# Kernel optimization log

Hardware: AMD Instinct MI355X
Metric: run time of the kernel (lower is better)

Reference implementation:

```python
import jax, jax.numpy as jnp
import numpy as np

N_HEADS = 8


def setup_inputs() -> dict:
    key = jax.random.key(0)
    qkv = jax.random.normal(key, (4, 1536, 2048), dtype=jnp.float32)
    return {"qkv": qkv}


def reference(qkv) -> jnp.ndarray:
    bs, width, length = qkv.shape
    assert width % (3 * N_HEADS) == 0
    ch = width // (3 * N_HEADS)
    # [bs*H, 3*ch, T] -> split into q, k, v each [bs*H, ch, T]
    qkv_ = qkv.reshape(bs * N_HEADS, 3 * ch, length)
    q, k, v = qkv_[:, :ch], qkv_[:, ch:2 * ch], qkv_[:, 2 * ch:]
    scale = 1.0 / np.sqrt(np.sqrt(ch)).astype(np.float32)
    # scores [bs*H, T_q, T_k]
    weight = jnp.einsum('bct,bcs->bts', q * scale, k * scale)
    # NOTE: faithful to source — softmax over dim=1 (the query axis t), in float32
    weight = jax.nn.softmax(weight.astype(jnp.float32), axis=1).astype(weight.dtype)
    a = jnp.einsum('bts,bcs->bct', weight, v)  # [bs*H, ch, T]
    return a.reshape(bs, N_HEADS * ch, length)
```

## Files before the change

kernel.cpp:

```cpp
#include <hip/hip_runtime.h>
#include <hip/hip_bf16.h>


#define SEQ   2048
#define CHD   64
#define NHB   32
#define SCALE_QK 0.42466090f

typedef short bf16x8 __attribute__((ext_vector_type(8)));
typedef float f32x4  __attribute__((ext_vector_type(4)));
typedef float f32x16 __attribute__((ext_vector_type(16)));
typedef unsigned int   u32x4 __attribute__((ext_vector_type(4)));
typedef unsigned short us8   __attribute__((ext_vector_type(8)));

extern "C" __device__ float __ocml_native_exp2_f32(float);
#define EXP2(x) __ocml_native_exp2_f32(x)

__device__ __forceinline__ unsigned short f2bf(float f) {
    unsigned int u = __builtin_bit_cast(unsigned int, f);
    u += 0x7FFFu + ((u >> 16) & 1u);
    return (unsigned short)(u >> 16);
}

__device__ __forceinline__ void gl_lds16(const void* g, void* l) {
    __builtin_amdgcn_global_load_lds(
        (const __attribute__((address_space(1))) void*)g,
        (__attribute__((address_space(3))) void*)l, 16, 0, 0);
}

__device__ __forceinline__ unsigned cvtpk(float a, float b) {
    unsigned r;
    asm("v_cvt_pk_bf16_f32 %0, %1, %2" : "=v"(r) : "v"(a), "v"(b));
    return r;
}
__device__ __forceinline__ void plswap(unsigned &a, unsigned &b) {
    asm("v_permlane32_swap_b32 %0, %1" : "+v"(a), "+v"(b));
}

#define ZERO16 {0.f,0.f,0.f,0.f,0.f,0.f,0.f,0.f,0.f,0.f,0.f,0.f,0.f,0.f,0.f,0.f}

__global__ __launch_bounds__(256) void convert_qk(
    const float* __restrict__ qkv, unsigned short* __restrict__ Qt,
    unsigned short* __restrict__ Kt)
{
    __shared__ float Tl[64][129];
    const int bid = blockIdx.x;
    const int head = bid >> 4, t0 = (bid & 15) * 128;
    const int b = head >> 3, h = head & 7;
    const float* base = qkv + (size_t)(b * 1536 + h * 192) * SEQ;
    const int tid = threadIdx.x;
#pragma unroll
    for (int pp = 0; pp < 2; ++pp) {
        const float* src = base + (size_t)(pp ? CHD : 0) * SEQ;
        unsigned short* dst = (pp ? Kt : Qt) + (size_t)head * SEQ * CHD;
        if (pp) __syncthreads();
        for (int e = tid; e < 8192; e += 256) {
            int c = e >> 7, ti = e & 127;
            Tl[c][ti] = src[(size_t)c * SEQ + t0 + ti];
        }
        __syncthreads();
        for (int g = tid; g < 1024; g += 256) {
            int t = g >> 3, cg = g & 7;
            us8 u;
#pragma unroll
            for (int j = 0; j < 8; ++j) u[j] = f2bf(Tl[cg * 8 + j][t] * SCALE_QK);
            *(us8*)(dst + (size_t)(t0 + t) * 64 + ((cg * 8) ^ ((t & 7) << 3))) = u;
        }
    }
}

__global__ __launch_bounds__(512, 2) void stats10_kernel(
    const float* __restrict__ qkv, const unsigned short* __restrict__ Qt,
    const unsigned short* __restrict__ Kt, unsigned short* __restrict__ Vb)
{
    __shared__ __attribute__((aligned(16))) unsigned short Qs[4][4096];
    __shared__ float rlb[256];
    const int bid = blockIdx.x;
    const int bs  = ((bid & 7) << 5) | (bid >> 3);
    const int head = bs >> 3, s0 = (bs & 7) * 256;
    const int b = head >> 3, h = head & 7;
    const char* Qhb = (const char*)(Qt + (size_t)head * SEQ * CHD);
    const unsigned short* Kh = Kt + (size_t)head * SEQ * CHD;
    const int tid = threadIdx.x, w = tid >> 6, l = tid & 63, lo5 = l & 31, hi = l >> 5;
    const int rsw = (lo5 & 7) << 3;

    bf16x8 kfr[4];
#pragma unroll
    for (int kc = 0; kc < 4; ++kc)
        kfr[kc] = *(const bf16x8*)(
            Kh + (size_t)(s0 + w * 32 + lo5) * 64 + (((kc << 4) + (hi << 3)) ^ rsw));

    auto stage = [&](int p, int tc) {
        gl_lds16(Qhb + (size_t)tc * 8192 + tid * 16, &Qs[p][0] + tid * 8);
    };

    float lacc[4] = {0.f, 0.f, 0.f, 0.f};

    stage(0, 0);
    stage(1, 1);
    for (int tc = 0; tc < 32; ++tc) {
        if (tc < 31) asm volatile("s_waitcnt vmcnt(1)" ::: "memory");
        else         asm volatile("s_waitcnt vmcnt(0)" ::: "memory");
        __builtin_amdgcn_s_barrier();
        __builtin_amdgcn_sched_barrier(0);
        if (tc < 30) stage((tc + 2) & 3, tc + 2);
        const unsigned short* qs = &Qs[tc & 3][0];
        __builtin_amdgcn_s_setprio(1);
#pragma unroll
        for (int ts = 0; ts < 2; ++ts) {
            f32x16 s = ZERO16;
#pragma unroll
            for (int kc = 0; kc < 4; ++kc) {
                bf16x8 qa = *(const bf16x8*)(
                    qs + (ts * 32 + lo5) * 64 + (((kc << 4) + (hi << 3)) ^ rsw));
                s = __builtin_amdgcn_mfma_f32_32x32x16_bf16(qa, kfr[kc], s, 0, 0, 0);
            }
#pragma unroll
            for (int r = 0; r < 16; ++r) lacc[r & 3] += EXP2(s[r]);
        }
        __builtin_amdgcn_s_setprio(0);
    }

    float lsum = (lacc[0] + lacc[1]) + (lacc[2] + lacc[3]);
    lsum += __shfl_xor(lsum, 32);
    if (l < 32) rlb[w * 32 + lo5] = 1.0f / lsum;
    __syncthreads();

    const float* vp = qkv + (size_t)(b * 1536 + h * 192 + 2 * CHD) * SEQ;
    unsigned short* Vh = Vb + (size_t)head * SEQ * CHD;
    for (int g = tid; g < 2048; g += 512) {
        int c = g >> 5, si8 = (g & 31) * 8;
        const float* vrow = vp + (size_t)c * SEQ + s0 + si8;
        f32x4 v0 = *(const f32x4*)(vrow);
        f32x4 v1 = *(const f32x4*)(vrow + 4);
        us8 u;
#pragma unroll
        for (int j = 0; j < 4; ++j) u[j]     = f2bf(v0[j] * rlb[si8 + j]);
#pragma unroll
        for (int j = 0; j < 4; ++j) u[4 + j] = f2bf(v1[j] * rlb[si8 + 4 + j]);
        int swb = (si8 & ~63) | ((si8 & 63) ^ ((c & 7) << 3));
        *(us8*)(Vh + (size_t)c * SEQ + s0 + swb) = u;
    }
}

__global__ __launch_bounds__(512, 2) void attn8_kernel(
    const unsigned short* __restrict__ Qt, const unsigned short* __restrict__ Kt,
    const unsigned short* __restrict__ Vb, float* __restrict__ out)
{
    __shared__ __attribute__((aligned(16))) unsigned short KV[4][8192];
    const int bid = blockIdx.x;
    const int bs  = ((bid & 7) << 5) | (bid >> 3);
    const int head = bs >> 3, t0 = (bs & 7) * 256;
    const int b = head >> 3, h = head & 7;
    const int tid = threadIdx.x, w = tid >> 6, l = tid & 63, lo5 = l & 31, hi = l >> 5;
    const int rsw = (lo5 & 7) << 3;
    const unsigned short* Qh = Qt + (size_t)head * SEQ * CHD;
    const char* Khb = (const char*)(Kt + (size_t)head * SEQ * CHD);
    const char* Vhb = (const char*)(Vb + (size_t)head * SEQ * CHD);
    const int tmine = t0 + w * 32 + lo5;

    bf16x8 qf[4];
#pragma unroll
    for (int kc = 0; kc < 4; ++kc)
        qf[kc] = *(const bf16x8*)(Qh + (size_t)tmine * 64 + (((kc << 4) + (hi << 3)) ^ rsw));

    f32x16 acc[2] = {ZERO16, ZERO16};

    const int vc = tid >> 3, vs16 = (tid & 7) * 16;
    auto stage = [&](int p, int cj) {
        unsigned short* kb = &KV[p][0];
        unsigned short* vb = &KV[p][4096];
        gl_lds16(Khb + (size_t)cj * 8192 + tid * 16, kb + tid * 8);
        gl_lds16(Vhb + (size_t)vc * 4096 + (size_t)cj * 128 + vs16,
                 vb + tid * 8);
    };

    stage(0, 0);
    stage(1, 1);

    for (int j = 0; j < 32; ++j) {
        const int p = j & 3;
        if (j < 31) asm volatile("s_waitcnt vmcnt(2)" ::: "memory");
        else        asm volatile("s_waitcnt vmcnt(0)" ::: "memory");
        __builtin_amdgcn_s_barrier();
        __builtin_amdgcn_sched_barrier(0);
        if (j < 30) stage((j + 2) & 3, j + 2);

        const unsigned short* kb = &KV[p][0];
        const unsigned short* vb = &KV[p][4096];
        bf16x8 vf[8];
#pragma unroll
        for (int ct = 0; ct < 2; ++ct)
#pragma unroll
            for (int ks = 0; ks < 4; ++ks)
                vf[ct * 4 + ks] = *(const bf16x8*)(
                    vb + (ct * 32 + lo5) * 64 + (((ks << 4) + (hi << 3)) ^ rsw));

        __builtin_amdgcn_s_setprio(1);
#pragma unroll
        for (int st = 0; st < 2; ++st) {
            f32x16 sacc = ZERO16;
#pragma unroll
            for (int kc = 0; kc < 4; ++kc) {
                bf16x8 kf = *(const bf16x8*)(
                    kb + (st * 32 + lo5) * 64 + (((kc << 4) + (hi << 3)) ^ rsw));
                sacc = __builtin_amdgcn_mfma_f32_32x32x16_bf16(kf, qf[kc], sacc, 0, 0, 0);
            }
            float p16[16];
#pragma unroll
            for (int r = 0; r < 16; ++r) p16[r] = EXP2(sacc[r]);
            unsigned w0 = cvtpk(p16[0],  p16[1]),  w1 = cvtpk(p16[2],  p16[3]);
            unsigned w2 = cvtpk(p16[4],  p16[5]),  w3 = cvtpk(p16[6],  p16[7]);
            unsigned w4 = cvtpk(p16[8],  p16[9]),  w5 = cvtpk(p16[10], p16[11]);
            unsigned w6 = cvtpk(p16[12], p16[13]), w7 = cvtpk(p16[14], p16[15]);
            plswap(w0, w2); plswap(w1, w3); plswap(w4, w6); plswap(w5, w7);
            bf16x8 pfA = __builtin_bit_cast(bf16x8, (u32x4){w0, w1, w2, w3});
            bf16x8 pfB = __builtin_bit_cast(bf16x8, (u32x4){w4, w5, w6, w7});
#pragma unroll
            for (int ct = 0; ct < 2; ++ct) {
                acc[ct] = __builtin_amdgcn_mfma_f32_32x32x16_bf16(vf[ct * 4 + st * 2 + 0], pfA, acc[ct], 0, 0, 0);
                acc[ct] = __builtin_amdgcn_mfma_f32_32x32x16_bf16(vf[ct * 4 + st * 2 + 1], pfB, acc[ct], 0, 0, 0);
            }
        }
        __builtin_amdgcn_s_setprio(0);
    }

    float* op = out + (size_t)(b * 512 + h * 64) * SEQ;
#pragma unroll
    for (int ct = 0; ct < 2; ++ct)
#pragma unroll
        for (int r = 0; r < 16; ++r) {
            int c = ct * 32 + (r & 3) + 8 * (r >> 2) + 4 * hi;
            op[(size_t)c * SEQ + tmine] = acc[ct][r];
        }
}


__device__ __forceinline__ bf16x8 lds_frag(const unsigned short* base, int row, int el) {
    int e = el ^ ((row & 7) << 3);
    return *(const bf16x8*)(base + row * 64 + e);
}

__global__ __launch_bounds__(256) void qkv_stats_kernel(
    const float* __restrict__ qkv, float* __restrict__ m_ws, float* __restrict__ rl_ws)
{
    __shared__ __attribute__((aligned(16))) unsigned short Kl[128 * 64];
    __shared__ __attribute__((aligned(16))) unsigned short Ql[64 * 64];
    const int head = blockIdx.x >> 4, stile = blockIdx.x & 15, s0 = stile * 128;
    const int b = head >> 3, h = head & 7;
    const float* qp = qkv + (size_t)(b * 1536 + h * 192) * SEQ;
    const float* kp = qp + (size_t)CHD * SEQ;
    const int tid = threadIdx.x, w = tid >> 6, l = tid & 63, lg = l >> 4, lr = l & 15;
    for (int idx = tid; idx < 128 * 64; idx += 256) {
        int s = idx & 127, c = idx >> 7;
        Kl[s * 64 + (c ^ ((s & 7) << 3))] = f2bf(kp[(size_t)c * SEQ + s0 + s]);
    }
    float m_run[2] = {-__builtin_inff(), -__builtin_inff()};
    float l_run[2] = {0.f, 0.f};
    for (int chunk = 0; chunk < 32; ++chunk) {
        const int t0 = chunk * 64;
        __syncthreads();
        for (int idx = tid; idx < 64 * 64; idx += 256) {
            int t = idx & 63, c = idx >> 6;
            Ql[t * 64 + (c ^ ((t & 7) << 3))] = f2bf(qp[(size_t)c * SEQ + t0 + t]);
        }
        __syncthreads();
#pragma unroll
        for (int ntl = 0; ntl < 2; ++ntl) {
            const int srow = 16 * (2 * w + ntl) + lr;
            float vals[16];
#pragma unroll
            for (int mt = 0; mt < 4; ++mt) {
                f32x4 sacc = {0.f, 0.f, 0.f, 0.f};
#pragma unroll
                for (int kk = 0; kk < 2; ++kk) {
                    bf16x8 a  = lds_frag(Ql, 16 * mt + lr, 32 * kk + 8 * lg);
                    bf16x8 bk = lds_frag(Kl, srow,         32 * kk + 8 * lg);
                    sacc = __builtin_amdgcn_mfma_f32_16x16x32_bf16(a, bk, sacc, 0, 0, 0);
                }
#pragma unroll
                for (int j = 0; j < 4; ++j) vals[mt * 4 + j] = sacc[j] * 0.125f;
            }
            float cm = vals[0];
#pragma unroll
            for (int i = 1; i < 16; ++i) cm = fmaxf(cm, vals[i]);
            cm = fmaxf(cm, __shfl_xor(cm, 16));
            cm = fmaxf(cm, __shfl_xor(cm, 32));
            float newm = fmaxf(m_run[ntl], cm);
            l_run[ntl] *= __expf(m_run[ntl] - newm);
            m_run[ntl] = newm;
            float ps = 0.f;
#pragma unroll
            for (int i = 0; i < 16; ++i) ps += __expf(vals[i] - newm);
            ps += __shfl_xor(ps, 16);
            ps += __shfl_xor(ps, 32);
            l_run[ntl] += ps;
        }
    }
    if (lg == 0) {
#pragma unroll
        for (int ntl = 0; ntl < 2; ++ntl) {
            int sg = s0 + 16 * (2 * w + ntl) + lr;
            m_ws[head * SEQ + sg]  = m_run[ntl];
            rl_ws[head * SEQ + sg] = 1.0f / l_run[ntl];
        }
    }
}

__global__ __launch_bounds__(256) void qkv_attn_kernel(
    const float* __restrict__ qkv, const float* __restrict__ m_ws,
    const float* __restrict__ rl_ws, float* __restrict__ out)
{
    __shared__ __attribute__((aligned(16))) unsigned short Ql[128 * 64];
    __shared__ __attribute__((aligned(16))) unsigned short Kl[64 * 64];
    __shared__ __attribute__((aligned(16))) unsigned short Vl[64 * 64];
    __shared__ __attribute__((aligned(16))) unsigned short Pl[128 * 64];
    const int head = blockIdx.x >> 4, ttile = blockIdx.x & 15, t0 = ttile * 128;
    const int b = head >> 3, h = head & 7;
    const float* qp  = qkv + (size_t)(b * 1536 + h * 192) * SEQ;
    const float* kp  = qp + (size_t)CHD * SEQ;
    const float* vp  = qp + (size_t)(2 * CHD) * SEQ;
    const float* mh  = m_ws  + head * SEQ;
    const float* rlh = rl_ws + head * SEQ;
    const int tid = threadIdx.x, w = tid >> 6, l = tid & 63, lg = l >> 4, lr = l & 15;
    for (int idx = tid; idx < 128 * 64; idx += 256) {
        int t = idx & 127, c = idx >> 7;
        Ql[t * 64 + (c ^ ((t & 7) << 3))] = f2bf(qp[(size_t)c * SEQ + t0 + t]);
    }
    f32x4 acc[4][2];
#pragma unroll
    for (int i = 0; i < 4; ++i)
#pragma unroll
        for (int j = 0; j < 2; ++j) acc[i][j] = (f32x4){0.f, 0.f, 0.f, 0.f};
    for (int sc = 0; sc < 32; ++sc) {
        const int s0 = sc * 64;
        __syncthreads();
        for (int idx = tid; idx < 64 * 64; idx += 256) {
            int s = idx & 63, c = idx >> 6;
            Kl[s * 64 + (c ^ ((s & 7) << 3))] = f2bf(kp[(size_t)c * SEQ + s0 + s]);
            Vl[c * 64 + (s ^ ((c & 7) << 3))] = f2bf(vp[(size_t)c * SEQ + s0 + s] * rlh[s0 + s]);
        }
        __syncthreads();
        float msv[4];
#pragma unroll
        for (int nts = 0; nts < 4; ++nts) msv[nts] = mh[s0 + 16 * nts + lr];
#pragma unroll
        for (int mts = 0; mts < 2; ++mts) {
            const int trowbase = 16 * (2 * w + mts);
#pragma unroll
            for (int nts = 0; nts < 4; ++nts) {
                f32x4 sa = {0.f, 0.f, 0.f, 0.f};
#pragma unroll
                for (int kk = 0; kk < 2; ++kk) {
                    bf16x8 a  = lds_frag(Ql, trowbase + lr, 32 * kk + 8 * lg);
                    bf16x8 bk = lds_frag(Kl, 16 * nts + lr, 32 * kk + 8 * lg);
                    sa = __builtin_amdgcn_mfma_f32_16x16x32_bf16(a, bk, sa, 0, 0, 0);
                }
                const int scol = 16 * nts + lr;
#pragma unroll
                for (int j = 0; j < 4; ++j) {
                    int trow = trowbase + 4 * lg + j;
                    float p = __expf(sa[j] * 0.125f - msv[nts]);
                    Pl[trow * 64 + (scol ^ ((trow & 7) << 3))] = f2bf(p);
                }
            }
        }
#pragma unroll
        for (int mt = 0; mt < 4; ++mt) {
#pragma unroll
            for (int ntl = 0; ntl < 2; ++ntl) {
                const int trow = 16 * (2 * w + ntl);
#pragma unroll
                for (int kk = 0; kk < 2; ++kk) {
                    bf16x8 a  = lds_frag(Vl, 16 * mt + lr, 32 * kk + 8 * lg);
                    bf16x8 bp = lds_frag(Pl, trow + lr,    32 * kk + 8 * lg);
                    acc[mt][ntl] = __builtin_amdgcn_mfma_f32_16x16x32_bf16(a, bp, acc[mt][ntl], 0, 0, 0);
                }
            }
        }
    }
    float* op = out + (size_t)(b * 512 + h * 64) * SEQ;
#pragma unroll
    for (int mt = 0; mt < 4; ++mt) {
#pragma unroll
        for (int ntl = 0; ntl < 2; ++ntl) {
            int tcol = t0 + 16 * (2 * w + ntl) + lr;
#pragma unroll
            for (int j = 0; j < 4; ++j) {
                int c = 16 * mt + 4 * lg + j;
                op[(size_t)c * SEQ + tcol] = acc[mt][ntl][j];
            }
        }
    }
}

extern "C" void kernel_launch(void* const* d_in, const int* in_sizes, int n_in,
                              void* d_out, int out_size, void* d_ws, size_t ws_size,
                              hipStream_t stream) {
    const float* qkv = (const float*)d_in[0];
    float* out = (float*)d_out;
    (void)in_sizes; (void)n_in; (void)out_size;

    const size_t need = (size_t)3 * NHB * SEQ * CHD * 2;
    if (ws_size >= need) {
        unsigned short* Qt = (unsigned short*)d_ws;
        unsigned short* Kt = Qt + (size_t)NHB * SEQ * CHD;
        unsigned short* Vb = Kt + (size_t)NHB * SEQ * CHD;
        convert_qk    <<<dim3(NHB * 16), dim3(256), 0, stream>>>(qkv, Qt, Kt);
        stats10_kernel<<<dim3(256),      dim3(512), 0, stream>>>(qkv, Qt, Kt, Vb);
        attn8_kernel  <<<dim3(NHB * 8),  dim3(512), 0, stream>>>(Qt, Kt, Vb, out);
    } else {
        float* m_ws  = (float*)d_ws;
        float* rl_ws = m_ws + (size_t)NHB * SEQ;
        qkv_stats_kernel<<<dim3(NHB * 16), dim3(256), 0, stream>>>(qkv, m_ws, rl_ws);
        qkv_attn_kernel <<<dim3(NHB * 16), dim3(256), 0, stream>>>(qkv, m_ws, rl_ws, out);
    }
}
```

Measured before the change: 85.05 us.

## Split key chunk across wave pairs with two query tiles per wave and LDS reduction

Each wave now handles two 32-query tiles and half of every 64-key chunk, instead of one query tile and the full chunk. K fragments are reused across both query tiles and each wave loads only half the V fragments, cutting LDS reads per MFMA. Partial P·V accumulators from each wave pair are summed through LDS at the end. Launch bounds drop to one block per CU to make room for the extra accumulators and Q fragments, which may reduce occupancy and latency hiding.

```diff
diff --git a/kernel.cpp b/kernel.cpp
--- a/kernel.cpp
+++ b/kernel.cpp
@@ -143,7 +143,7 @@
     }
 }
 
-__global__ __launch_bounds__(512, 2) void attn8_kernel(
+__global__ __launch_bounds__(512, 1) void attn13_kernel(
     const unsigned short* __restrict__ Qt, const unsigned short* __restrict__ Kt,
     const unsigned short* __restrict__ Vb, float* __restrict__ out)
 {
@@ -153,26 +153,29 @@
     const int head = bs >> 3, t0 = (bs & 7) * 256;
     const int b = head >> 3, h = head & 7;
     const int tid = threadIdx.x, w = tid >> 6, l = tid & 63, lo5 = l & 31, hi = l >> 5;
+    const int tw = w >> 1, sh = w & 1;
     const int rsw = (lo5 & 7) << 3;
     const unsigned short* Qh = Qt + (size_t)head * SEQ * CHD;
     const char* Khb = (const char*)(Kt + (size_t)head * SEQ * CHD);
     const char* Vhb = (const char*)(Vb + (size_t)head * SEQ * CHD);
-    const int tmine = t0 + w * 32 + lo5;
-
-    bf16x8 qf[4];
-#pragma unroll
-    for (int kc = 0; kc < 4; ++kc)
-        qf[kc] = *(const bf16x8*)(Qh + (size_t)tmine * 64 + (((kc << 4) + (hi << 3)) ^ rsw));
-
-    f32x16 acc[2] = {ZERO16, ZERO16};
+
+    bf16x8 qfA[4], qfB[4];
+#pragma unroll
+    for (int kc = 0; kc < 4; ++kc) {
+        qfA[kc] = *(const bf16x8*)(
+            Qh + (size_t)(t0 + tw * 64 + lo5) * 64 + (((kc << 4) + (hi << 3)) ^ rsw));
+        qfB[kc] = *(const bf16x8*)(
+            Qh + (size_t)(t0 + tw * 64 + 32 + lo5) * 64 + (((kc << 4) + (hi << 3)) ^ rsw));
+    }
+
+    f32x16 accA0 = ZERO16, accA1 = ZERO16, accB0 = ZERO16, accB1 = ZERO16;
 
     const int vc = tid >> 3, vs16 = (tid & 7) * 16;
     auto stage = [&](int p, int cj) {
         unsigned short* kb = &KV[p][0];
         unsigned short* vb = &KV[p][4096];
         gl_lds16(Khb + (size_t)cj * 8192 + tid * 16, kb + tid * 8);
-        gl_lds16(Vhb + (size_t)vc * 4096 + (size_t)cj * 128 + vs16,
-                 vb + tid * 8);
+        gl_lds16(Vhb + (size_t)vc * 4096 + (size_t)cj * 128 + vs16, vb + tid * 8);
     };
 
     stage(0, 0);
@@ -188,27 +191,30 @@
 
         const unsigned short* kb = &KV[p][0];
         const unsigned short* vb = &KV[p][4096];
-        bf16x8 vf[8];
-#pragma unroll
-        for (int ct = 0; ct < 2; ++ct)
-#pragma unroll
-            for (int ks = 0; ks < 4; ++ks)
-                vf[ct * 4 + ks] = *(const bf16x8*)(
-                    vb + (ct * 32 + lo5) * 64 + (((ks << 4) + (hi << 3)) ^ rsw));
+
+        bf16x8 kf[4], vf0k0, vf0k1, vf1k0, vf1k1;
+#pragma unroll
+        for (int kc = 0; kc < 4; ++kc)
+            kf[kc] = *(const bf16x8*)(
+                kb + (sh * 32 + lo5) * 64 + (((kc << 4) + (hi << 3)) ^ rsw));
+        vf0k0 = *(const bf16x8*)(vb + (lo5) * 64       + ((sh * 32 +      (hi << 3)) ^ rsw));
+        vf0k1 = *(const bf16x8*)(vb + (lo5) * 64       + ((sh * 32 + 16 + (hi << 3)) ^ rsw));
+        vf1k0 = *(const bf16x8*)(vb + (32 + lo5) * 64  + ((sh * 32 +      (hi << 3)) ^ rsw));
+        vf1k1 = *(const bf16x8*)(vb + (32 + lo5) * 64  + ((sh * 32 + 16 + (hi << 3)) ^ rsw));
 
         __builtin_amdgcn_s_setprio(1);
-#pragma unroll
-        for (int st = 0; st < 2; ++st) {
-            f32x16 sacc = ZERO16;
-#pragma unroll
-            for (int kc = 0; kc < 4; ++kc) {
-                bf16x8 kf = *(const bf16x8*)(
-                    kb + (st * 32 + lo5) * 64 + (((kc << 4) + (hi << 3)) ^ rsw));
-                sacc = __builtin_amdgcn_mfma_f32_32x32x16_bf16(kf, qf[kc], sacc, 0, 0, 0);
-            }
+        f32x16 SA = ZERO16, SB = ZERO16;
+#pragma unroll
+        for (int kc = 0; kc < 4; ++kc)
+            SA = __builtin_amdgcn_mfma_f32_32x32x16_bf16(kf[kc], qfA[kc], SA, 0, 0, 0);
+#pragma unroll
+        for (int kc = 0; kc < 4; ++kc)
+            SB = __builtin_amdgcn_mfma_f32_32x32x16_bf16(kf[kc], qfB[kc], SB, 0, 0, 0);
+
+        {
             float p16[16];
 #pragma unroll
-            for (int r = 0; r < 16; ++r) p16[r] = EXP2(sacc[r]);
+            for (int r = 0; r < 16; ++r) p16[r] = EXP2(SA[r]);
             unsigned w0 = cvtpk(p16[0],  p16[1]),  w1 = cvtpk(p16[2],  p16[3]);
             unsigned w2 = cvtpk(p16[4],  p16[5]),  w3 = cvtpk(p16[6],  p16[7]);
             unsigned w4 = cvtpk(p16[8],  p16[9]),  w5 = cvtpk(p16[10], p16[11]);
@@ -216,23 +222,54 @@
             plswap(w0, w2); plswap(w1, w3); plswap(w4, w6); plswap(w5, w7);
             bf16x8 pfA = __builtin_bit_cast(bf16x8, (u32x4){w0, w1, w2, w3});
             bf16x8 pfB = __builtin_bit_cast(bf16x8, (u32x4){w4, w5, w6, w7});
-#pragma unroll
-            for (int ct = 0; ct < 2; ++ct) {
-                acc[ct] = __builtin_amdgcn_mfma_f32_32x32x16_bf16(vf[ct * 4 + st * 2 + 0], pfA, acc[ct], 0, 0, 0);
-                acc[ct] = __builtin_amdgcn_mfma_f32_32x32x16_bf16(vf[ct * 4 + st * 2 + 1], pfB, acc[ct], 0, 0, 0);
-            }
+            accA0 = __builtin_amdgcn_mfma_f32_32x32x16_bf16(vf0k0, pfA, accA0, 0, 0, 0);
+            accA0 = __builtin_amdgcn_mfma_f32_32x32x16_bf16(vf0k1, pfB, accA0, 0, 0, 0);
+            accA1 = __builtin_amdgcn_mfma_f32_32x32x16_bf16(vf1k0, pfA, accA1, 0, 0, 0);
+            accA1 = __builtin_amdgcn_mfma_f32_32x32x16_bf16(vf1k1, pfB, accA1, 0, 0, 0);
+        }
+        {
+            float p16[16];
+#pragma unroll
+            for (int r = 0; r < 16; ++r) p16[r] = EXP2(SB[r]);
+            unsigned w0 = cvtpk(p16[0],  p16[1]),  w1 = cvtpk(p16[2],  p16[3]);
+            unsigned w2 = cvtpk(p16[4],  p16[5]),  w3 = cvtpk(p16[6],  p16[7]);
+            unsigned w4 = cvtpk(p16[8],  p16[9]),  w5 = cvtpk(p16[10], p16[11]);
+            unsigned w6 = cvtpk(p16[12], p16[13]), w7 = cvtpk(p16[14], p16[15]);
+            plswap(w0, w2); plswap(w1, w3); plswap(w4, w6); plswap(w5, w7);
+            bf16x8 pfA = __builtin_bit_cast(bf16x8, (u32x4){w0, w1, w2, w3});
+            bf16x8 pfB = __builtin_bit_cast(bf16x8, (u32x4){w4, w5, w6, w7});
+            accB0 = __builtin_amdgcn_mfma_f32_32x32x16_bf16(vf0k0, pfA, accB0, 0, 0, 0);
+            accB0 = __builtin_amdgcn_mfma_f32_32x32x16_bf16(vf0k1, pfB, accB0, 0, 0, 0);
+            accB1 = __builtin_amdgcn_mfma_f32_32x32x16_bf16(vf1k0, pfA, accB1, 0, 0, 0);
+            accB1 = __builtin_amdgcn_mfma_f32_32x32x16_bf16(vf1k1, pfB, accB1, 0, 0, 0);
         }
         __builtin_amdgcn_s_setprio(0);
     }
 
+    __syncthreads();
+    float* red = (float*)&KV[0][0];
+    if (sh == 0) {
+        *(f32x16*)(red + (size_t)w * 2048 + l * 16)        = accA1;
+        *(f32x16*)(red + (size_t)w * 2048 + 1024 + l * 16) = accB1;
+    } else {
+        *(f32x16*)(red + (size_t)w * 2048 + l * 16)        = accA0;
+        *(f32x16*)(red + (size_t)w * 2048 + 1024 + l * 16) = accB0;
+    }
+    __syncthreads();
+    f32x16 pA = *(const f32x16*)(red + (size_t)(w ^ 1) * 2048 + l * 16);
+    f32x16 pB = *(const f32x16*)(red + (size_t)(w ^ 1) * 2048 + 1024 + l * 16);
+    f32x16 finA, finB;
+    if (sh == 0) { finA = accA0 + pA; finB = accB0 + pB; }
+    else         { finA = accA1 + pA; finB = accB1 + pB; }
+
     float* op = out + (size_t)(b * 512 + h * 64) * SEQ;
-#pragma unroll
-    for (int ct = 0; ct < 2; ++ct)
-#pragma unroll
-        for (int r = 0; r < 16; ++r) {
-            int c = ct * 32 + (r & 3) + 8 * (r >> 2) + 4 * hi;
-            op[(size_t)c * SEQ + tmine] = acc[ct][r];
-        }
+    const int tA = t0 + tw * 64 + lo5, tB = tA + 32;
+#pragma unroll
+    for (int r = 0; r < 16; ++r) {
+        int c = sh * 32 + (r & 3) + 8 * (r >> 2) + 4 * hi;
+        op[(size_t)c * SEQ + tA] = finA[r];
+        op[(size_t)c * SEQ + tB] = finB[r];
+    }
 }
 
 
@@ -408,7 +445,7 @@
         unsigned short* Vb = Kt + (size_t)NHB * SEQ * CHD;
         convert_qk    <<<dim3(NHB * 16), dim3(256), 0, stream>>>(qkv, Qt, Kt);
         stats10_kernel<<<dim3(256),      dim3(512), 0, stream>>>(qkv, Qt, Kt, Vb);
-        attn8_kernel  <<<dim3(NHB * 8),  dim3(512), 0, stream>>>(Qt, Kt, Vb, out);
+        attn13_kernel <<<dim3(256),      dim3(512), 0, stream>>>(Qt, Kt, Vb, out);
     } else {
         float* m_ws  = (float*)d_ws;
         float* rl_ws = m_ws + (size_t)NHB * SEQ;
```

New measurement: 82.80 us (median of 3 runs). 2.6% less time.

## Split stats and attention work across twice as many blocks with atomic/LDS reductions

Applied to the files above, without the earlier changes.

The column-sum stats kernel is split into two halves over the query axis, with partial sums combined via atomic adds into a zeroed workspace. A separate small kernel then applies the reciprocal and converts V to bf16. The attention kernel now uses 128-query tiles with waves splitting the key chunk in two, reducing partial outputs through LDS. This doubles the grid size to fill more CUs, at the cost of an extra memset, an extra launch, atomics and a final LDS reduction.

```diff
diff --git a/kernel.cpp b/kernel.cpp
--- a/kernel.cpp
+++ b/kernel.cpp
@@ -69,66 +69,78 @@
     }
 }
 
-__global__ __launch_bounds__(512, 2) void stats10_kernel(
-    const float* __restrict__ qkv, const unsigned short* __restrict__ Qt,
-    const unsigned short* __restrict__ Kt, unsigned short* __restrict__ Vb)
+__global__ __launch_bounds__(512, 4) void statsA_kernel(
+    const unsigned short* __restrict__ Qt, const unsigned short* __restrict__ Kt,
+    float* __restrict__ l_ws)
 {
     __shared__ __attribute__((aligned(16))) unsigned short Qs[4][4096];
+    const int bid = blockIdx.x;
+    const int bs  = ((bid & 7) << 6) | (bid >> 3);
+    const int head = bs >> 4, s0 = ((bs >> 1) & 7) * 256, tH = bs & 1;
+    const char* Qhb = (const char*)(Qt + (size_t)head * SEQ * CHD);
+    const unsigned short* Kh = Kt + (size_t)head * SEQ * CHD;
+    const int tid = threadIdx.x, w = tid >> 6, l = tid & 63, lo5 = l & 31, hi = l >> 5;
+    const int rsw = (lo5 & 7) << 3;
+
+    bf16x8 kfr[4];
+#pragma unroll
+    for (int kc = 0; kc < 4; ++kc)
+        kfr[kc] = *(const bf16x8*)(
+            Kh + (size_t)(s0 + w * 32 + lo5) * 64 + (((kc << 4) + (hi << 3)) ^ rsw));
+
+    auto stage = [&](int p, int tc) {
+        gl_lds16(Qhb + (size_t)(tH * 16 + tc) * 8192 + tid * 16, &Qs[p][0] + tid * 8);
+    };
+
+    float lacc[4] = {0.f, 0.f, 0.f, 0.f};
+
+    stage(0, 0);
+    stage(1, 1);
+    for (int tc = 0; tc < 16; ++tc) {
+        if (tc < 15) asm volatile("s_waitcnt vmcnt(1)" ::: "memory");
+        else         asm volatile("s_waitcnt vmcnt(0)" ::: "memory");
+        __builtin_amdgcn_s_barrier();
+        __builtin_amdgcn_sched_barrier(0);
+        if (tc < 14) stage((tc + 2) & 3, tc + 2);
+        const unsigned short* qs = &Qs[tc & 3][0];
+        __builtin_amdgcn_s_setprio(1);
+#pragma unroll
+        for (int ts = 0; ts < 2; ++ts) {
+            f32x16 s = ZERO16;
+#pragma unroll
+            for (int kc = 0; kc < 4; ++kc) {
+                bf16x8 qa = *(const bf16x8*)(
+                    qs + (ts * 32 + lo5) * 64 + (((kc << 4) + (hi << 3)) ^ rsw));
+                s = __builtin_amdgcn_mfma_f32_32x32x16_bf16(qa, kfr[kc], s, 0, 0, 0);
+            }
+#pragma unroll
+            for (int r = 0; r < 16; ++r) lacc[r & 3] += EXP2(s[r]);
+        }
+        __builtin_amdgcn_s_setprio(0);
+    }
+
+    float lsum = (lacc[0] + lacc[1]) + (lacc[2] + lacc[3]);
+    lsum += __shfl_xor(lsum, 32);
+    if (l < 32) unsafeAtomicAdd(&l_ws[head * SEQ + s0 + w * 32 + lo5], lsum);
+}
+
+__global__ __launch_bounds__(256) void statsB_kernel(
+    const float* __restrict__ qkv, const float* __restrict__ l_ws,
+    unsigned short* __restrict__ Vb)
+{
     __shared__ float rlb[256];
     const int bid = blockIdx.x;
     const int bs  = ((bid & 7) << 5) | (bid >> 3);
     const int head = bs >> 3, s0 = (bs & 7) * 256;
     const int b = head >> 3, h = head & 7;
-    const char* Qhb = (const char*)(Qt + (size_t)head * SEQ * CHD);
-    const unsigned short* Kh = Kt + (size_t)head * SEQ * CHD;
-    const int tid = threadIdx.x, w = tid >> 6, l = tid & 63, lo5 = l & 31, hi = l >> 5;
-    const int rsw = (lo5 & 7) << 3;
-
-    bf16x8 kfr[4];
-#pragma unroll
-    for (int kc = 0; kc < 4; ++kc)
-        kfr[kc] = *(const bf16x8*)(
-            Kh + (size_t)(s0 + w * 32 + lo5) * 64 + (((kc << 4) + (hi << 3)) ^ rsw));
-
-    auto stage = [&](int p, int tc) {
-        gl_lds16(Qhb + (size_t)tc * 8192 + tid * 16, &Qs[p][0] + tid * 8);
-    };
-
-    float lacc[4] = {0.f, 0.f, 0.f, 0.f};
-
-    stage(0, 0);
-    stage(1, 1);
-    for (int tc = 0; tc < 32; ++tc) {
-        if (tc < 31) asm volatile("s_waitcnt vmcnt(1)" ::: "memory");
-        else         asm volatile("s_waitcnt vmcnt(0)" ::: "memory");
-        __builtin_amdgcn_s_barrier();
-        __builtin_amdgcn_sched_barrier(0);
-        if (tc < 30) stage((tc + 2) & 3, tc + 2);
-        const unsigned short* qs = &Qs[tc & 3][0];
-        __builtin_amdgcn_s_setprio(1);
-#pragma unroll
-        for (int ts = 0; ts < 2; ++ts) {
-            f32x16 s = ZERO16;
-#pragma unroll
-            for (int kc = 0; kc < 4; ++kc) {
-                bf16x8 qa = *(const bf16x8*)(
-                    qs + (ts * 32 + lo5) * 64 + (((kc << 4) + (hi << 3)) ^ rsw));
-                s = __builtin_amdgcn_mfma_f32_32x32x16_bf16(qa, kfr[kc], s, 0, 0, 0);
-            }
-#pragma unroll
-            for (int r = 0; r < 16; ++r) lacc[r & 3] += EXP2(s[r]);
-        }
-        __builtin_amdgcn_s_setprio(0);
-    }
-
-    float lsum = (lacc[0] + lacc[1]) + (lacc[2] + lacc[3]);
-    lsum += __shfl_xor(lsum, 32);
-    if (l < 32) rlb[w * 32 + lo5] = 1.0f / lsum;
+    const int tid = threadIdx.x;
+
+    rlb[tid] = 1.0f / l_ws[head * SEQ + s0 + tid];
     __syncthreads();
 
     const float* vp = qkv + (size_t)(b * 1536 + h * 192 + 2 * CHD) * SEQ;
     unsigned short* Vh = Vb + (size_t)head * SEQ * CHD;
-    for (int g = tid; g < 2048; g += 512) {
+    for (int g = tid; g < 2048; g += 256) {
         int c = g >> 5, si8 = (g & 31) * 8;
         const float* vrow = vp + (size_t)c * SEQ + s0 + si8;
         f32x4 v0 = *(const f32x4*)(vrow);
@@ -143,21 +155,22 @@
     }
 }
 
-__global__ __launch_bounds__(512, 2) void attn8_kernel(
+__global__ __launch_bounds__(512, 4) void attn9x_kernel(
     const unsigned short* __restrict__ Qt, const unsigned short* __restrict__ Kt,
     const unsigned short* __restrict__ Vb, float* __restrict__ out)
 {
-    __shared__ __attribute__((aligned(16))) unsigned short KV[4][8192];
+    __shared__ __attribute__((aligned(16))) unsigned short KV[3][8192];
     const int bid = blockIdx.x;
-    const int bs  = ((bid & 7) << 5) | (bid >> 3);
-    const int head = bs >> 3, t0 = (bs & 7) * 256;
+    const int bs  = ((bid & 7) << 6) | (bid >> 3);
+    const int head = bs >> 4, t0 = (bs & 15) * 128;
     const int b = head >> 3, h = head & 7;
     const int tid = threadIdx.x, w = tid >> 6, l = tid & 63, lo5 = l & 31, hi = l >> 5;
+    const int tsub = w >> 1, sh = w & 1;
     const int rsw = (lo5 & 7) << 3;
     const unsigned short* Qh = Qt + (size_t)head * SEQ * CHD;
     const char* Khb = (const char*)(Kt + (size_t)head * SEQ * CHD);
     const char* Vhb = (const char*)(Vb + (size_t)head * SEQ * CHD);
-    const int tmine = t0 + w * 32 + lo5;
+    const int tmine = t0 + tsub * 32 + lo5;
 
     bf16x8 qf[4];
 #pragma unroll
@@ -171,68 +184,71 @@
         unsigned short* kb = &KV[p][0];
         unsigned short* vb = &KV[p][4096];
         gl_lds16(Khb + (size_t)cj * 8192 + tid * 16, kb + tid * 8);
-        gl_lds16(Vhb + (size_t)vc * 4096 + (size_t)cj * 128 + vs16,
-                 vb + tid * 8);
+        gl_lds16(Vhb + (size_t)vc * 4096 + (size_t)cj * 128 + vs16, vb + tid * 8);
     };
 
     stage(0, 0);
     stage(1, 1);
 
     for (int j = 0; j < 32; ++j) {
-        const int p = j & 3;
+        const int p = j % 3;
         if (j < 31) asm volatile("s_waitcnt vmcnt(2)" ::: "memory");
         else        asm volatile("s_waitcnt vmcnt(0)" ::: "memory");
         __builtin_amdgcn_s_barrier();
         __builtin_amdgcn_sched_barrier(0);
-        if (j < 30) stage((j + 2) & 3, j + 2);
+        if (j < 30) stage((j + 2) % 3, j + 2);
 
         const unsigned short* kb = &KV[p][0];
         const unsigned short* vb = &KV[p][4096];
-        bf16x8 vf[8];
+        bf16x8 kf[4], vf[4];
+#pragma unroll
+        for (int kc = 0; kc < 4; ++kc)
+            kf[kc] = *(const bf16x8*)(
+                kb + (sh * 32 + lo5) * 64 + (((kc << 4) + (hi << 3)) ^ rsw));
 #pragma unroll
         for (int ct = 0; ct < 2; ++ct)
 #pragma unroll
-            for (int ks = 0; ks < 4; ++ks)
-                vf[ct * 4 + ks] = *(const bf16x8*)(
-                    vb + (ct * 32 + lo5) * 64 + (((ks << 4) + (hi << 3)) ^ rsw));
+            for (int ks = 0; ks < 2; ++ks)
+                vf[ct * 2 + ks] = *(const bf16x8*)(
+                    vb + (ct * 32 + lo5) * 64 +
+                    (((sh * 32 + ks * 16 + (hi << 3))) ^ rsw));
 
         __builtin_amdgcn_s_setprio(1);
-#pragma unroll
-        for (int st = 0; st < 2; ++st) {
-            f32x16 sacc = ZERO16;
-#pragma unroll
-            for (int kc = 0; kc < 4; ++kc) {
-                bf16x8 kf = *(const bf16x8*)(
-                    kb + (st * 32 + lo5) * 64 + (((kc << 4) + (hi << 3)) ^ rsw));
-                sacc = __builtin_amdgcn_mfma_f32_32x32x16_bf16(kf, qf[kc], sacc, 0, 0, 0);
-            }
-            float p16[16];
-#pragma unroll
-            for (int r = 0; r < 16; ++r) p16[r] = EXP2(sacc[r]);
-            unsigned w0 = cvtpk(p16[0],  p16[1]),  w1 = cvtpk(p16[2],  p16[3]);
-            unsigned w2 = cvtpk(p16[4],  p16[5]),  w3 = cvtpk(p16[6],  p16[7]);
-            unsigned w4 = cvtpk(p16[8],  p16[9]),  w5 = cvtpk(p16[10], p16[11]);
-            unsigned w6 = cvtpk(p16[12], p16[13]), w7 = cvtpk(p16[14], p16[15]);
-            plswap(w0, w2); plswap(w1, w3); plswap(w4, w6); plswap(w5, w7);
-            bf16x8 pfA = __builtin_bit_cast(bf16x8, (u32x4){w0, w1, w2, w3});
-            bf16x8 pfB = __builtin_bit_cast(bf16x8, (u32x4){w4, w5, w6, w7});
-#pragma unroll
-            for (int ct = 0; ct < 2; ++ct) {
-                acc[ct] = __builtin_amdgcn_mfma_f32_32x32x16_bf16(vf[ct * 4 + st * 2 + 0], pfA, acc[ct], 0, 0, 0);
-                acc[ct] = __builtin_amdgcn_mfma_f32_32x32x16_bf16(vf[ct * 4 + st * 2 + 1], pfB, acc[ct], 0, 0, 0);
-            }
+        f32x16 sacc = ZERO16;
+#pragma unroll
+        for (int kc = 0; kc < 4; ++kc)
+            sacc = __builtin_amdgcn_mfma_f32_32x32x16_bf16(kf[kc], qf[kc], sacc, 0, 0, 0);
+        float p16[16];
+#pragma unroll
+        for (int r = 0; r < 16; ++r) p16[r] = EXP2(sacc[r]);
+        unsigned w0 = cvtpk(p16[0],  p16[1]),  w1 = cvtpk(p16[2],  p16[3]);
+        unsigned w2 = cvtpk(p16[4],  p16[5]),  w3 = cvtpk(p16[6],  p16[7]);
+        unsigned w4 = cvtpk(p16[8],  p16[9]),  w5 = cvtpk(p16[10], p16[11]);
+        unsigned w6 = cvtpk(p16[12], p16[13]), w7 = cvtpk(p16[14], p16[15]);
+        plswap(w0, w2); plswap(w1, w3); plswap(w4, w6); plswap(w5, w7);
+        bf16x8 pfA = __builtin_bit_cast(bf16x8, (u32x4){w0, w1, w2, w3});
+        bf16x8 pfB = __builtin_bit_cast(bf16x8, (u32x4){w4, w5, w6, w7});
+#pragma unroll
+        for (int ct = 0; ct < 2; ++ct) {
+            acc[ct] = __builtin_amdgcn_mfma_f32_32x32x16_bf16(vf[ct * 2 + 0], pfA, acc[ct], 0, 0, 0);
+            acc[ct] = __builtin_amdgcn_mfma_f32_32x32x16_bf16(vf[ct * 2 + 1], pfB, acc[ct], 0, 0, 0);
         }
         __builtin_amdgcn_s_setprio(0);
     }
 
+    __syncthreads();
+    float* red = (float*)&KV[0][0];
+    *(f32x16*)(red + (size_t)w * 1024 + l * 16) = acc[sh ^ 1];
+    __syncthreads();
+    f32x16 peer = *(const f32x16*)(red + (size_t)(w ^ 1) * 1024 + l * 16);
+    f32x16 fin = acc[sh] + peer;
+
     float* op = out + (size_t)(b * 512 + h * 64) * SEQ;
 #pragma unroll
-    for (int ct = 0; ct < 2; ++ct)
-#pragma unroll
-        for (int r = 0; r < 16; ++r) {
-            int c = ct * 32 + (r & 3) + 8 * (r >> 2) + 4 * hi;
-            op[(size_t)c * SEQ + tmine] = acc[ct][r];
-        }
+    for (int r = 0; r < 16; ++r) {
+        int c = sh * 32 + (r & 3) + 8 * (r >> 2) + 4 * hi;
+        op[(size_t)c * SEQ + tmine] = fin[r];
+    }
 }
 
 
@@ -401,14 +417,18 @@
     float* out = (float*)d_out;
     (void)in_sizes; (void)n_in; (void)out_size;
 
-    const size_t need = (size_t)3 * NHB * SEQ * CHD * 2;
+    const size_t bufE = (size_t)NHB * SEQ * CHD;
+    const size_t need = 3 * bufE * 2 + (size_t)NHB * SEQ * 4;
     if (ws_size >= need) {
         unsigned short* Qt = (unsigned short*)d_ws;
-        unsigned short* Kt = Qt + (size_t)NHB * SEQ * CHD;
-        unsigned short* Vb = Kt + (size_t)NHB * SEQ * CHD;
-        convert_qk    <<<dim3(NHB * 16), dim3(256), 0, stream>>>(qkv, Qt, Kt);
-        stats10_kernel<<<dim3(256),      dim3(512), 0, stream>>>(qkv, Qt, Kt, Vb);
-        attn8_kernel  <<<dim3(NHB * 8),  dim3(512), 0, stream>>>(Qt, Kt, Vb, out);
+        unsigned short* Kt = Qt + bufE;
+        unsigned short* Vb = Kt + bufE;
+        float* l_ws = (float*)(Vb + bufE);
+        hipMemsetAsync(l_ws, 0, (size_t)NHB * SEQ * 4, stream);
+        convert_qk   <<<dim3(NHB * 16), dim3(256), 0, stream>>>(qkv, Qt, Kt);
+        statsA_kernel<<<dim3(512),      dim3(512), 0, stream>>>(Qt, Kt, l_ws);
+        statsB_kernel<<<dim3(256),      dim3(256), 0, stream>>>(qkv, l_ws, Vb);
+        attn9x_kernel<<<dim3(NHB * 16), dim3(512), 0, stream>>>(Qt, Kt, Vb, out);
     } else {
         float* m_ws  = (float*)d_ws;
         float* rl_ws = m_ws + (size_t)NHB * SEQ;
```

New measurement: 97.72 us. +14.9%, slower.
